# Kernel tuning notes

Measured on AMD Instinct MI355X. Metric: run time of the kernel, lower is better.

Reference implementation:

```python
import jax, jax.numpy as jnp
import numpy as np

B, N, F, D, KVQ, H, S, ITERS = 64, 4096, 256, 256, 256, 4, 8, 3
DH = KVQ // H
SCALE = DH ** -0.5
EPS = 1e-8
LN_EPS = 1e-5


def layernorm(x, w, b):
    m = jnp.mean(x, axis=-1, keepdims=True)
    v = jnp.var(x, axis=-1, keepdims=True)
    return (x - m) * jax.lax.rsqrt(v + LN_EPS) * w + b


def setup_inputs() -> dict:
    key = jax.random.key(0)
    ks = jax.random.split(key, 8)
    def init(k, shape, fan_in):
        return jax.random.normal(k, shape, dtype=jnp.float32) * (fan_in ** -0.5)
    return {
        "inputs": jax.random.normal(ks[0], (B, N, F), dtype=jnp.float32),
        "conditioning": jax.random.normal(ks[1], (B, S, D), dtype=jnp.float32),
        "ln_in_w": jnp.ones((F,), jnp.float32),
        "ln_in_b": jnp.zeros((F,), jnp.float32),
        "ln_s_w": jnp.ones((D,), jnp.float32),
        "ln_s_b": jnp.zeros((D,), jnp.float32),
        "wq": init(ks[2], (KVQ, D), D),
        "wk": init(ks[3], (KVQ, F), F),
        "wv": init(ks[4], (KVQ, F), F),
        "gru_wih": init(ks[5], (3 * D, KVQ), KVQ),
        "gru_whh": init(ks[6], (3 * D, D), D),
        "gru_bih": jnp.zeros((3 * D,), jnp.float32),
        "gru_bhh": jnp.zeros((3 * D,), jnp.float32),
    }


def gru_cell(x, h, wih, whh, bih, bhh):
    # x: [..., KVQ], h: [..., D]; torch.nn.GRUCell math
    gi = x @ wih.T + bih  # [..., 3D]
    gh = h @ whh.T + bhh
    i_r, i_z, i_n = jnp.split(gi, 3, axis=-1)
    h_r, h_z, h_n = jnp.split(gh, 3, axis=-1)
    r = jax.nn.sigmoid(i_r + h_r)
    z = jax.nn.sigmoid(i_z + h_z)
    n = jnp.tanh(i_n + r * h_n)
    return (1.0 - z) * n + z * h


def reference(inputs, conditioning, ln_in_w, ln_in_b, ln_s_w, ln_s_b, wq, wk, wv, gru_wih, gru_whh, gru_bih, gru_bhh):
    x = layernorm(inputs, ln_in_w, ln_in_b)  # [B,N,F]
    k = (x @ wk.T).reshape(B, N, H, DH)
    v = (x @ wv.T).reshape(B, N, H, DH)

    slots = conditioning
    attn_out = None
    for _ in range(ITERS):
        slots_prev = slots
        sn = layernorm(slots, ln_s_w, ln_s_b)
        q = (sn @ wq.T).reshape(B, S, H, DH)
        dots = jnp.einsum('bihd,bjhd->bihj', q, k) * SCALE  # [B,S,H,N]
        # inverted softmax: normalize over flattened (slot, head) axis
        attn = jax.nn.softmax(dots.reshape(B, S * H, N), axis=1).reshape(B, S, H, N)
        attn_before = attn
        attn = attn + EPS
        attn = attn / jnp.sum(attn, axis=-1, keepdims=True)
        updates = jnp.einsum('bjhd,bihj->bihd', v, attn).reshape(B, S, KVQ)
        slots = gru_cell(updates.reshape(-1, KVQ), slots_prev.reshape(-1, D),
                         gru_wih, gru_whh, gru_bih, gru_bhh).reshape(B, S, D)
        attn_out = jnp.mean(attn_before, axis=2)  # [B,S,N]
    return slots, attn_out
```

## Files before the change

kernel.cpp:

```cpp
#include <hip/hip_runtime.h>
#include <hip/hip_bf16.h>
#include <math.h>


using frag_ab = __attribute__((ext_vector_type(8))) short;
using f32x4  = __attribute__((ext_vector_type(4))) float;

__device__ __forceinline__ unsigned short f2bf(float f) {
  unsigned int x = __float_as_uint(f);
  x += 0x7fffu + ((x >> 16) & 1u);
  return (unsigned short)(x >> 16);
}
__device__ __forceinline__ float bf2f(unsigned short u) {
  return __uint_as_float((unsigned int)u << 16);
}
__device__ __forceinline__ float dot8(const uint4 w, const float* __restrict__ x) {
  return bf2f((unsigned short)(w.x & 0xffff)) * x[0] +
         bf2f((unsigned short)(w.x >> 16)) * x[1] +
         bf2f((unsigned short)(w.y & 0xffff)) * x[2] +
         bf2f((unsigned short)(w.y >> 16)) * x[3] +
         bf2f((unsigned short)(w.z & 0xffff)) * x[4] +
         bf2f((unsigned short)(w.z >> 16)) * x[5] +
         bf2f((unsigned short)(w.w & 0xffff)) * x[6] +
         bf2f((unsigned short)(w.w >> 16)) * x[7];
}

__global__ __launch_bounds__(256) void k_wcvt2(const float* __restrict__ wih,
                                               const float* __restrict__ whh,
                                               const float* __restrict__ wv,
                                               unsigned short* __restrict__ wihB,
                                               unsigned short* __restrict__ whhB,
                                               unsigned short* __restrict__ wvB) {
  const long idx = (long)blockIdx.x * 1024 + threadIdx.x * 4;
  const float* src;
  unsigned short* dst;
  long off;
  if (idx < 196608) { src = wih; dst = wihB; off = idx; }
  else if (idx < 393216) { src = whh; dst = whhB; off = idx - 196608; }
  else { src = wv; dst = wvB; off = idx - 393216; }
  const float4 v = *(const float4*)(src + off);
  uint2 o;
  o.x = (unsigned)f2bf(v.x) | ((unsigned)f2bf(v.y) << 16);
  o.y = (unsigned)f2bf(v.z) | ((unsigned)f2bf(v.w) << 16);
  *(uint2*)(dst + off) = o;
}

__global__ __launch_bounds__(256) void k_mprep(const float* __restrict__ wq,
                                               const float* __restrict__ wk,
                                               unsigned short* __restrict__ MTB) {
  const int f = blockIdx.x, h = blockIdx.y, D = threadIdx.x;
  float acc = 0.f;
#pragma unroll 8
  for (int d = 0; d < 64; ++d)
    acc += wq[(h * 64 + d) * 256 + D] * wk[(h * 64 + d) * 256 + f];
  MTB[((long)(h * 256 + f)) * 256 + D] = f2bf(acc * 0.125f);
}

__global__ __launch_bounds__(256) void k_precvt(
    const float* __restrict__ xsrc, const float* __restrict__ lnw,
    const float* __restrict__ lnb, unsigned short* __restrict__ Xh,
    unsigned short* __restrict__ XhT) {
  __shared__ __align__(16) unsigned short XT[256 * 68];
  const int t = threadIdx.x;
  const int lane = t & 63, w = t >> 6;
  const long row0 = (long)blockIdx.x * 64;
  const long b = row0 >> 12;
  const long j0 = row0 & 4095;

  float w4[4], b4[4];
#pragma unroll
  for (int k = 0; k < 4; ++k) {
    w4[k] = lnw[k * 64 + lane];
    b4[k] = lnb[k * 64 + lane];
  }
  for (int rr = 0; rr < 16; ++rr) {
    const long row = row0 + w * 16 + rr;
    float x[4];
    float s = 0.f, ss = 0.f;
#pragma unroll
    for (int k = 0; k < 4; ++k) {
      x[k] = xsrc[row * 256 + k * 64 + lane];
      s += x[k];
      ss += x[k] * x[k];
    }
#pragma unroll
    for (int m = 1; m < 64; m <<= 1) {
      s += __shfl_xor(s, m);
      ss += __shfl_xor(ss, m);
    }
    const float mean = s * (1.f / 256.f);
    const float rstd = rsqrtf(ss * (1.f / 256.f) - mean * mean + 1e-5f);
#pragma unroll
    for (int k = 0; k < 4; ++k) {
      const unsigned short u = f2bf((x[k] - mean) * rstd * w4[k] + b4[k]);
      Xh[row * 256 + k * 64 + lane] = u;
      *(unsigned short*)((char*)XT + (k * 64 + lane) * 136 + (w * 16 + rr) * 2) = u;
    }
  }
  __syncthreads();
#pragma unroll
  for (int fp = 0; fp < 4; ++fp) {
    const int f = fp * 64 + (t >> 2);
    const int jq = t & 3;
    uint2 v0 = *(const uint2*)((const char*)XT + f * 136 + jq * 32 + 0);
    uint2 v1 = *(const uint2*)((const char*)XT + f * 136 + jq * 32 + 8);
    uint2 v2 = *(const uint2*)((const char*)XT + f * 136 + jq * 32 + 16);
    uint2 v3 = *(const uint2*)((const char*)XT + f * 136 + jq * 32 + 24);
    unsigned short* dst = XhT + (b * 256 + f) * 4096 + j0 + jq * 16;
    *(uint4*)(dst) = make_uint4(v0.x, v0.y, v1.x, v1.y);
    *(uint4*)(dst + 8) = make_uint4(v2.x, v2.y, v3.x, v3.y);
  }
}

__global__ __launch_bounds__(256) void k_sv(const unsigned short* __restrict__ XhT,
                                            float* __restrict__ svx) {
  const int b = blockIdx.x >> 2, fq = blockIdx.x & 3;
  const int lane = threadIdx.x & 63, w = threadIdx.x >> 6;
  for (int rr = 0; rr < 16; ++rr) {
    const int f = fq * 64 + w * 16 + rr;
    const unsigned short* p = XhT + ((long)(b * 256 + f)) * 4096;
    float s = 0.f;
#pragma unroll
    for (int i = 0; i < 8; ++i) {
      const uint4 v = *(const uint4*)(p + i * 512 + lane * 8);
      s += bf2f((unsigned short)(v.x & 0xffff)) + bf2f((unsigned short)(v.x >> 16)) +
           bf2f((unsigned short)(v.y & 0xffff)) + bf2f((unsigned short)(v.y >> 16)) +
           bf2f((unsigned short)(v.z & 0xffff)) + bf2f((unsigned short)(v.z >> 16)) +
           bf2f((unsigned short)(v.w & 0xffff)) + bf2f((unsigned short)(v.w >> 16));
    }
#pragma unroll
    for (int m = 1; m < 64; m <<= 1) s += __shfl_xor(s, m);
    if (lane == 0) svx[b * 256 + f] = s;
  }
}

__global__ __launch_bounds__(256) void k_q(
    const float* __restrict__ slots, const float* __restrict__ lnw,
    const float* __restrict__ lnb, const unsigned short* __restrict__ MTB,
    unsigned short* __restrict__ qt) {
  __shared__ float sl[8 * 256];
  __shared__ float mstat[8], rstat[8];
  const int b = blockIdx.x, h = blockIdx.y, t = threadIdx.x;
#pragma unroll
  for (int i = 0; i < 8; ++i) sl[i * 256 + t] = slots[b * 2048 + i * 256 + t];
  __syncthreads();
  if (t < 8) {
    float s = 0.f, ss = 0.f;
    for (int k = 0; k < 256; ++k) {
      const float x = sl[t * 256 + k];
      s += x;
      ss += x * x;
    }
    const float m = s * (1.f / 256.f);
    mstat[t] = m;
    rstat[t] = rsqrtf(ss * (1.f / 256.f) - m * m + 1e-5f);
  }
  __syncthreads();
  const float w = lnw[t], bb = lnb[t];
#pragma unroll
  for (int i = 0; i < 8; ++i)
    sl[i * 256 + t] = (sl[i * 256 + t] - mstat[i]) * rstat[i] * w + bb;
  __syncthreads();
  float acc[8] = {};
  const uint4* mrow = (const uint4*)(MTB + ((long)(h * 256 + t)) * 256);
#pragma unroll 4
  for (int D8 = 0; D8 < 32; ++D8) {
    const uint4 m = mrow[D8];
#pragma unroll
    for (int i = 0; i < 8; ++i) acc[i] += dot8(m, sl + i * 256 + D8 * 8);
  }
#pragma unroll
  for (int i = 0; i < 8; ++i) {
    const int ih = i * 4 + h;
    *(unsigned short*)((char*)qt + b * 16384 + ih * 512 +
                       ((2 * t) ^ ((ih & 7) << 4))) = f2bf(acc[i]);
  }
}

template <bool LAST>
__global__ __launch_bounds__(256) void k_att(
    const unsigned short* __restrict__ qt, const unsigned short* __restrict__ Xh,
    const unsigned short* __restrict__ XhT, float* __restrict__ upart,
    float* __restrict__ rowsum_part, float* __restrict__ attn_out) {
  __shared__ __align__(16) unsigned short Qs[32 * 256];
  __shared__ __align__(16) unsigned short Ps[4][1024];
  __shared__ float ured[4][2048];
  __shared__ float wred[4][32];
  const int t = threadIdx.x;
  const int lane = t & 63, wid = t >> 6;
  const int li = lane & 15, kg = lane >> 4;
  const int b = blockIdx.y;
  const long j0 = (long)blockIdx.x * 512 + wid * 128;

#pragma unroll
  for (int rnd = 0; rnd < 4; ++rnd)
    __builtin_amdgcn_global_load_lds(
        (const unsigned int*)((const char*)qt + b * 16384 + rnd * 4096 + t * 16),
        (unsigned int*)((char*)Qs + rnd * 4096 + t * 16), 16, 0, 0);
  __syncthreads();

  float rsum0 = 0.f, rsum1 = 0.f;
  f32x4 pv[2][16];
#pragma unroll
  for (int s = 0; s < 2; ++s)
#pragma unroll
    for (int ft = 0; ft < 16; ++ft) pv[s][ft] = (f32x4){0.f, 0.f, 0.f, 0.f};

  unsigned short* Pw = Ps[wid];

  for (int ch = 0; ch < 4; ++ch) {
    const long jc = j0 + ch * 32;
    f32x4 dacc[2][2];
    dacc[0][0] = (f32x4){0.f, 0.f, 0.f, 0.f};
    dacc[0][1] = (f32x4){0.f, 0.f, 0.f, 0.f};
    dacc[1][0] = (f32x4){0.f, 0.f, 0.f, 0.f};
    dacc[1][1] = (f32x4){0.f, 0.f, 0.f, 0.f};
#pragma unroll
    for (int jsub = 0; jsub < 2; ++jsub) {
      frag_ab kf[8];
      const unsigned short* kp =
          Xh + ((long)b * 4096 + jc + jsub * 16 + li) * 256 + kg * 8;
#pragma unroll
      for (int ks = 0; ks < 8; ++ks) kf[ks] = *(const frag_ab*)(kp + ks * 32);
#pragma unroll
      for (int g = 0; g < 2; ++g) {
        const char* qrow = (const char*)Qs + (g * 16 + li) * 512;
        const int swz = (li & 7) << 4;
#pragma unroll
        for (int ks = 0; ks < 8; ++ks) {
          const frag_ab qf = *(const frag_ab*)(qrow + ((ks * 64 + kg * 16) ^ swz));
          dacc[jsub][g] = __builtin_amdgcn_mfma_f32_16x16x32_bf16(
              kf[ks], qf, dacc[jsub][g], 0, 0, 0);
        }
      }
    }
    float p[2][2][4];
#pragma unroll
    for (int jsub = 0; jsub < 2; ++jsub) {
#pragma unroll
      for (int r = 0; r < 4; ++r) {
        const float d0 = dacc[jsub][0][r];
        const float d1 = dacc[jsub][1][r];
        float mx = fmaxf(d0, d1);
        mx = fmaxf(mx, __shfl_xor(mx, 1));
        mx = fmaxf(mx, __shfl_xor(mx, 2));
        mx = fmaxf(mx, __shfl_xor(mx, 4));
        mx = fmaxf(mx, __shfl_xor(mx, 8));
        float e0 = __expf(d0 - mx), e1 = __expf(d1 - mx);
        float sm = e0 + e1;
        sm += __shfl_xor(sm, 1);
        sm += __shfl_xor(sm, 2);
        sm += __shfl_xor(sm, 4);
        sm += __shfl_xor(sm, 8);
        const float inv = 1.f / sm;
        e0 *= inv;
        e1 *= inv;
        p[jsub][0][r] = e0;
        p[jsub][1][r] = e1;
        rsum0 += e0;
        rsum1 += e1;
        if (LAST) {
          float s0 = e0 + __shfl_xor(e0, 1);
          s0 += __shfl_xor(s0, 2);
          float s1 = e1 + __shfl_xor(e1, 1);
          s1 += __shfl_xor(s1, 2);
          if ((li & 3) == 0) {
            const long jg = jc + jsub * 16 + kg * 4 + r;
            attn_out[((long)b * 8 + (li >> 2)) * 4096 + jg] = s0 * 0.25f;
            attn_out[((long)b * 8 + 4 + (li >> 2)) * 4096 + jg] = s1 * 0.25f;
          }
        }
      }
    }
    asm volatile("s_waitcnt lgkmcnt(0)" ::: "memory");
#pragma unroll
    for (int g = 0; g < 2; ++g) {
      const int ih = g * 16 + li;
      char* prow = (char*)Pw + ih * 64;
      const int swz = ((ih >> 2) & 3) << 4;
#pragma unroll
      for (int jsub = 0; jsub < 2; ++jsub)
#pragma unroll
        for (int rp = 0; rp < 2; ++rp) {
          const unsigned int pk =
              (unsigned)f2bf(p[jsub][g][2 * rp]) |
              ((unsigned)f2bf(p[jsub][g][2 * rp + 1]) << 16);
          const int jb = (jsub * 16 + kg * 4 + 2 * rp) * 2;
          *(unsigned int*)(prow + (jb ^ swz)) = pk;
        }
    }
    asm volatile("s_waitcnt lgkmcnt(0)" ::: "memory");
    const frag_ab pa0 = *(const frag_ab*)(
        (const char*)Pw + li * 64 + ((kg * 16) ^ (((li >> 2) & 3) << 4)));
    const frag_ab pa1 = *(const frag_ab*)(
        (const char*)Pw + (16 + li) * 64 +
        ((kg * 16) ^ ((((16 + li) >> 2) & 3) << 4)));
#pragma unroll
    for (int ft = 0; ft < 16; ++ft) {
      const frag_ab vf = *(const frag_ab*)(
          XhT + ((long)b * 256 + ft * 16 + li) * 4096 + jc + kg * 8);
      pv[0][ft] = __builtin_amdgcn_mfma_f32_16x16x32_bf16(pa0, vf, pv[0][ft], 0, 0, 0);
      pv[1][ft] = __builtin_amdgcn_mfma_f32_16x16x32_bf16(pa1, vf, pv[1][ft], 0, 0, 0);
    }
  }

  rsum0 += __shfl_xor(rsum0, 16);
  rsum0 += __shfl_xor(rsum0, 32);
  rsum1 += __shfl_xor(rsum1, 16);
  rsum1 += __shfl_xor(rsum1, 32);
  if (lane < 16) {
    wred[wid][lane] = rsum0;
    wred[wid][16 + lane] = rsum1;
  }

  const long pb = (long)blockIdx.x * 64 + b;
#pragma unroll
  for (int p4 = 0; p4 < 4; ++p4) {
    __syncthreads();
    if ((kg >> 1) == (p4 & 1)) {
#pragma unroll
      for (int ft = 0; ft < 16; ++ft)
#pragma unroll
        for (int r = 0; r < 4; ++r)
          ured[wid][((kg & 1) * 4 + r) * 256 + ft * 16 + li] = pv[p4 >> 1][ft][r];
    }
    __syncthreads();
#pragma unroll
    for (int o = 0; o < 8; ++o) {
      const int idx = o * 256 + t;
      upart[(pb * 32 + p4 * 8 + o) * 256 + t] =
          ured[0][idx] + ured[1][idx] + ured[2][idx] + ured[3][idx];
    }
  }
  if (t < 32)
    rowsum_part[pb * 32 + t] = wred[0][t] + wred[1][t] + wred[2][t] + wred[3][t];
}

__global__ __launch_bounds__(256) void k_xu(
    const float* __restrict__ upart, const float* __restrict__ svx,
    const float* __restrict__ rowsum_part, float* __restrict__ xu) {
  const int t = threadIdx.x;
  const int ih = blockIdx.x;
  const int b = blockIdx.y;
  float s2 = 0.f;
#pragma unroll
  for (int p = 0; p < 8; ++p)
    s2 += rowsum_part[((long)(p * 64 + b)) * 32 + ih];
  const float rs = 1.f / (s2 + 4096.f * 1e-8f);
  float pp = 0.f;
#pragma unroll
  for (int p = 0; p < 8; ++p)
    pp += upart[(((long)(p * 64 + b)) * 32 + ih) * 256 + t];
  xu[((long)(b * 32 + ih)) * 256 + t] = (pp + svx[b * 256 + t] * 1e-8f) * rs;
}

template <bool LAST>
__global__ __launch_bounds__(512, 4) void k_gq(
    const float* __restrict__ xu, const unsigned short* __restrict__ wvB,
    const unsigned short* __restrict__ wihB, const unsigned short* __restrict__ whhB,
    const float* __restrict__ bih, const float* __restrict__ bhh,
    const float* __restrict__ lnw, const float* __restrict__ lnb,
    const unsigned short* __restrict__ MTB, float* __restrict__ slots,
    unsigned short* __restrict__ qt, float* __restrict__ dout) {
  __shared__ float xul[4][256];
  __shared__ float hl[256];
  __shared__ float up2[2][256];
  __shared__ float updF[256];
  __shared__ float gI[3][256], gH[3][256];
  __shared__ float snl[256];
  __shared__ float mr[2];
  const int t = threadIdx.x;
  const int i = blockIdx.x;
  const int b = blockIdx.y;
  const int f = t & 255, half = t >> 8;

  if (t < 256) hl[t] = slots[b * 2048 + i * 256 + t];
#pragma unroll
  for (int hh = 0; hh < 2; ++hh) {
    const int row = half * 2 + hh;
    xul[row][f] = xu[((long)(b * 32 + i * 4 + row)) * 256 + f];
  }
  __syncthreads();
  {
    const float* xr = xul[f >> 6];
    const uint4* wr = (const uint4*)(wvB + (long)f * 256 + half * 128);
    float a = 0.f;
#pragma unroll 4
    for (int k8 = 0; k8 < 16; ++k8) a += dot8(wr[k8], xr + half * 128 + k8 * 8);
    up2[half][f] = a;
  }
  __syncthreads();
  if (t < 256) updF[t] = up2[0][t] + up2[1][t];
  __syncthreads();
  {
    const int c = t;
    const uint4* wi = (const uint4*)(wihB + (long)c * 256);
    const uint4* wh = (const uint4*)(whhB + (long)c * 256);
    float gi = 0.f, gh = 0.f;
#pragma unroll 4
    for (int k8 = 0; k8 < 32; ++k8) {
      gi += dot8(wi[k8], updF + k8 * 8);
      gh += dot8(wh[k8], hl + k8 * 8);
    }
    gI[c >> 8][c & 255] = gi + bih[c];
    gH[c >> 8][c & 255] = gh + bhh[c];
  }
  if (t < 256) {
    const int c = 512 + t;
    const uint4* wi = (const uint4*)(wihB + (long)c * 256);
    const uint4* wh = (const uint4*)(whhB + (long)c * 256);
    float gi = 0.f, gh = 0.f;
#pragma unroll 4
    for (int k8 = 0; k8 < 32; ++k8) {
      gi += dot8(wi[k8], updF + k8 * 8);
      gh += dot8(wh[k8], hl + k8 * 8);
    }
    gI[2][t] = gi + bih[c];
    gH[2][t] = gh + bhh[c];
  }
  __syncthreads();
  if (t < 256) {
    const float r = 1.f / (1.f + __expf(-(gI[0][t] + gH[0][t])));
    const float z = 1.f / (1.f + __expf(-(gI[1][t] + gH[1][t])));
    const float n = tanhf(gI[2][t] + r * gH[2][t]);
    const float hn = (1.f - z) * n + z * hl[t];
    slots[b * 2048 + i * 256 + t] = hn;
    if (LAST) dout[b * 2048 + i * 256 + t] = hn;
    xul[0][t] = hn;
  }
  if (LAST) return;
  __syncthreads();
  if (t < 64) {
    float s = 0.f, ss = 0.f;
#pragma unroll
    for (int u = 0; u < 4; ++u) {
      const float x = xul[0][u * 64 + t];
      s += x;
      ss += x * x;
    }
#pragma unroll
    for (int m = 1; m < 64; m <<= 1) {
      s += __shfl_xor(s, m);
      ss += __shfl_xor(ss, m);
    }
    if (t == 0) {
      const float mn = s * (1.f / 256.f);
      mr[0] = mn;
      mr[1] = rsqrtf(ss * (1.f / 256.f) - mn * mn + 1e-5f);
    }
  }
  __syncthreads();
  if (t < 256) snl[t] = (xul[0][t] - mr[0]) * mr[1] * lnw[t] + lnb[t];
  __syncthreads();
#pragma unroll
  for (int hh = 0; hh < 2; ++hh) {
    const int h = half * 2 + hh;
    const uint4* m = (const uint4*)(MTB + ((long)(h * 256 + f)) * 256);
    float acc = 0.f;
#pragma unroll 4
    for (int D8 = 0; D8 < 32; ++D8) acc += dot8(m[D8], snl + D8 * 8);
    const int ih = i * 4 + h;
    *(unsigned short*)((char*)qt + b * 16384 + ih * 512 +
                       ((2 * f) ^ ((ih & 7) << 4))) = f2bf(acc);
  }
}

extern "C" void kernel_launch(void* const* d_in, const int* in_sizes, int n_in,
                              void* d_out, int out_size, void* d_ws,
                              size_t ws_size, hipStream_t stream) {
  const float* xin = (const float*)d_in[0];
  const float* cond = (const float*)d_in[1];
  const float* lnin_w = (const float*)d_in[2];
  const float* lnin_b = (const float*)d_in[3];
  const float* lns_w = (const float*)d_in[4];
  const float* lns_b = (const float*)d_in[5];
  const float* wq = (const float*)d_in[6];
  const float* wk = (const float*)d_in[7];
  const float* wv = (const float*)d_in[8];
  const float* gwih = (const float*)d_in[9];
  const float* gwhh = (const float*)d_in[10];
  const float* gbih = (const float*)d_in[11];
  const float* gbhh = (const float*)d_in[12];
  float* out = (float*)d_out;

  char* ws = (char*)d_ws;
  unsigned short* Xh = (unsigned short*)ws;   ws += 262144l * 256 * 2;
  unsigned short* XhT = (unsigned short*)ws;  ws += 64l * 256 * 4096 * 2;
  unsigned short* MTB = (unsigned short*)ws;  ws += 4l * 256 * 256 * 2;
  unsigned short* qt = (unsigned short*)ws;   ws += 64l * 32 * 256 * 2;
  float* upart = (float*)ws;                  ws += 8l * 64 * 32 * 256 * 4;
  float* svx = (float*)ws;                    ws += 64l * 256 * 4;
  float* rowsum_part = (float*)ws;            ws += 8l * 64 * 32 * 4;
  float* xu = (float*)ws;                     ws += 64l * 32 * 256 * 4;
  float* slots = (float*)ws;                  ws += 512l * 256 * 4;
  unsigned short* wihB = (unsigned short*)ws; ws += 768l * 256 * 2;
  unsigned short* whhB = (unsigned short*)ws; ws += 768l * 256 * 2;
  unsigned short* wvB = (unsigned short*)ws;  ws += 256l * 256 * 2;

  hipMemcpyAsync(slots, cond, 512 * 256 * 4, hipMemcpyDeviceToDevice, stream);
  k_wcvt2<<<448, 256, 0, stream>>>(gwih, gwhh, wv, wihB, whhB, wvB);
  k_mprep<<<dim3(256, 4), 256, 0, stream>>>(wq, wk, MTB);
  k_precvt<<<4096, 256, 0, stream>>>(xin, lnin_w, lnin_b, Xh, XhT);
  k_sv<<<256, 256, 0, stream>>>(XhT, svx);
  k_q<<<dim3(64, 4), 256, 0, stream>>>(slots, lns_w, lns_b, MTB, qt);

  k_att<false><<<dim3(8, 64), 256, 0, stream>>>(qt, Xh, XhT, upart,
                                                rowsum_part, out + 131072);
  k_xu<<<dim3(32, 64), 256, 0, stream>>>(upart, svx, rowsum_part, xu);
  k_gq<false><<<dim3(8, 64), 512, 0, stream>>>(xu, wvB, wihB, whhB, gbih, gbhh,
                                               lns_w, lns_b, MTB, slots, qt, out);
  k_att<false><<<dim3(8, 64), 256, 0, stream>>>(qt, Xh, XhT, upart,
                                                rowsum_part, out + 131072);
  k_xu<<<dim3(32, 64), 256, 0, stream>>>(upart, svx, rowsum_part, xu);
  k_gq<false><<<dim3(8, 64), 512, 0, stream>>>(xu, wvB, wihB, whhB, gbih, gbhh,
                                               lns_w, lns_b, MTB, slots, qt, out);
  k_att<true><<<dim3(8, 64), 256, 0, stream>>>(qt, Xh, XhT, upart,
                                               rowsum_part, out + 131072);
  k_xu<<<dim3(32, 64), 256, 0, stream>>>(upart, svx, rowsum_part, xu);
  k_gq<true><<<dim3(8, 64), 512, 0, stream>>>(xu, wvB, wihB, whhB, gbih, gbhh,
                                              lns_w, lns_b, MTB, slots, qt, out);
}
```

Baseline: 655.1 us.

## Fuse column-sum into layernorm prepass and fold xu reduction into GRU kernel

The per-feature column sums of the normalized inputs are now accumulated inside the layernorm/transpose kernel as per-block partials. A tiny reduction kernel combines them, replacing a separate pass that re-read the whole transposed bf16 tensor. The k_xu kernel, launched once per iteration, is removed and its partial-sum reduction and normalization move into the GRU/query kernel, saving three launches and an intermediate buffer. tanhf is replaced with an exp-based approximation, and the column sums now come from fp32 values rather than bf16-rounded ones.

After: 629.0 us. 4.0% less time.

```diff
diff --git a/kernel.cpp b/kernel.cpp
--- a/kernel.cpp
+++ b/kernel.cpp
@@ -23,6 +23,11 @@
          bf2f((unsigned short)(w.z >> 16)) * x[5] +
          bf2f((unsigned short)(w.w & 0xffff)) * x[6] +
          bf2f((unsigned short)(w.w >> 16)) * x[7];
+}
+__device__ __forceinline__ float fast_tanh(float x) {
+  const float xc = fminf(fmaxf(x, -15.f), 15.f);
+  const float e2 = __expf(2.f * xc);
+  return (e2 - 1.f) / (e2 + 1.f);
 }
 
 __global__ __launch_bounds__(256) void k_wcvt2(const float* __restrict__ wih,
@@ -59,8 +64,9 @@
 __global__ __launch_bounds__(256) void k_precvt(
     const float* __restrict__ xsrc, const float* __restrict__ lnw,
     const float* __restrict__ lnb, unsigned short* __restrict__ Xh,
-    unsigned short* __restrict__ XhT) {
+    unsigned short* __restrict__ XhT, float* __restrict__ svp) {
   __shared__ __align__(16) unsigned short XT[256 * 68];
+  __shared__ float svred[4][256];
   const int t = threadIdx.x;
   const int lane = t & 63, w = t >> 6;
   const long row0 = (long)blockIdx.x * 64;
@@ -73,6 +79,7 @@
     w4[k] = lnw[k * 64 + lane];
     b4[k] = lnb[k * 64 + lane];
   }
+  float sacc[4] = {0.f, 0.f, 0.f, 0.f};
   for (int rr = 0; rr < 16; ++rr) {
     const long row = row0 + w * 16 + rr;
     float x[4];
@@ -92,12 +99,18 @@
     const float rstd = rsqrtf(ss * (1.f / 256.f) - mean * mean + 1e-5f);
 #pragma unroll
     for (int k = 0; k < 4; ++k) {
-      const unsigned short u = f2bf((x[k] - mean) * rstd * w4[k] + b4[k]);
+      const float xl = (x[k] - mean) * rstd * w4[k] + b4[k];
+      sacc[k] += xl;
+      const unsigned short u = f2bf(xl);
       Xh[row * 256 + k * 64 + lane] = u;
       *(unsigned short*)((char*)XT + (k * 64 + lane) * 136 + (w * 16 + rr) * 2) = u;
     }
   }
-  __syncthreads();
+#pragma unroll
+  for (int k = 0; k < 4; ++k) svred[w][k * 64 + lane] = sacc[k];
+  __syncthreads();
+  svp[(long)blockIdx.x * 256 + t] =
+      svred[0][t] + svred[1][t] + svred[2][t] + svred[3][t];
 #pragma unroll
   for (int fp = 0; fp < 4; ++fp) {
     const int f = fp * 64 + (t >> 2);
@@ -112,26 +125,13 @@
   }
 }
 
-__global__ __launch_bounds__(256) void k_sv(const unsigned short* __restrict__ XhT,
-                                            float* __restrict__ svx) {
-  const int b = blockIdx.x >> 2, fq = blockIdx.x & 3;
-  const int lane = threadIdx.x & 63, w = threadIdx.x >> 6;
-  for (int rr = 0; rr < 16; ++rr) {
-    const int f = fq * 64 + w * 16 + rr;
-    const unsigned short* p = XhT + ((long)(b * 256 + f)) * 4096;
-    float s = 0.f;
-#pragma unroll
-    for (int i = 0; i < 8; ++i) {
-      const uint4 v = *(const uint4*)(p + i * 512 + lane * 8);
-      s += bf2f((unsigned short)(v.x & 0xffff)) + bf2f((unsigned short)(v.x >> 16)) +
-           bf2f((unsigned short)(v.y & 0xffff)) + bf2f((unsigned short)(v.y >> 16)) +
-           bf2f((unsigned short)(v.z & 0xffff)) + bf2f((unsigned short)(v.z >> 16)) +
-           bf2f((unsigned short)(v.w & 0xffff)) + bf2f((unsigned short)(v.w >> 16));
-    }
-#pragma unroll
-    for (int m = 1; m < 64; m <<= 1) s += __shfl_xor(s, m);
-    if (lane == 0) svx[b * 256 + f] = s;
-  }
+__global__ __launch_bounds__(256) void k_svr(const float* __restrict__ svp,
+                                             float* __restrict__ svx) {
+  const int b = blockIdx.x, t = threadIdx.x;
+  float s = 0.f;
+#pragma unroll 8
+  for (int c = 0; c < 64; ++c) s += svp[((long)(b * 64 + c)) * 256 + t];
+  svx[b * 256 + t] = s;
 }
 
 __global__ __launch_bounds__(256) void k_q(
@@ -336,27 +336,10 @@
     rowsum_part[pb * 32 + t] = wred[0][t] + wred[1][t] + wred[2][t] + wred[3][t];
 }
 
-__global__ __launch_bounds__(256) void k_xu(
-    const float* __restrict__ upart, const float* __restrict__ svx,
-    const float* __restrict__ rowsum_part, float* __restrict__ xu) {
-  const int t = threadIdx.x;
-  const int ih = blockIdx.x;
-  const int b = blockIdx.y;
-  float s2 = 0.f;
-#pragma unroll
-  for (int p = 0; p < 8; ++p)
-    s2 += rowsum_part[((long)(p * 64 + b)) * 32 + ih];
-  const float rs = 1.f / (s2 + 4096.f * 1e-8f);
-  float pp = 0.f;
-#pragma unroll
-  for (int p = 0; p < 8; ++p)
-    pp += upart[(((long)(p * 64 + b)) * 32 + ih) * 256 + t];
-  xu[((long)(b * 32 + ih)) * 256 + t] = (pp + svx[b * 256 + t] * 1e-8f) * rs;
-}
-
 template <bool LAST>
 __global__ __launch_bounds__(512, 4) void k_gq(
-    const float* __restrict__ xu, const unsigned short* __restrict__ wvB,
+    const float* __restrict__ upart, const float* __restrict__ svx,
+    const float* __restrict__ rowsum_part, const unsigned short* __restrict__ wvB,
     const unsigned short* __restrict__ wihB, const unsigned short* __restrict__ whhB,
     const float* __restrict__ bih, const float* __restrict__ bhh,
     const float* __restrict__ lnw, const float* __restrict__ lnb,
@@ -375,10 +358,21 @@
   const int f = t & 255, half = t >> 8;
 
   if (t < 256) hl[t] = slots[b * 2048 + i * 256 + t];
+  const float svf = svx[b * 256 + f] * 1e-8f;
 #pragma unroll
   for (int hh = 0; hh < 2; ++hh) {
     const int row = half * 2 + hh;
-    xul[row][f] = xu[((long)(b * 32 + i * 4 + row)) * 256 + f];
+    const int ih = i * 4 + row;
+    float s2 = 0.f;
+#pragma unroll
+    for (int p = 0; p < 8; ++p)
+      s2 += rowsum_part[((long)(p * 64 + b)) * 32 + ih];
+    const float rs = 1.f / (s2 + 4096.f * 1e-8f);
+    float pp = 0.f;
+#pragma unroll
+    for (int p = 0; p < 8; ++p)
+      pp += upart[(((long)(p * 64 + b)) * 32 + ih) * 256 + f];
+    xul[row][f] = (pp + svf) * rs;
   }
   __syncthreads();
   {
@@ -422,7 +416,7 @@
   if (t < 256) {
     const float r = 1.f / (1.f + __expf(-(gI[0][t] + gH[0][t])));
     const float z = 1.f / (1.f + __expf(-(gI[1][t] + gH[1][t])));
-    const float n = tanhf(gI[2][t] + r * gH[2][t]);
+    const float n = fast_tanh(gI[2][t] + r * gH[2][t]);
     const float hn = (1.f - z) * n + z * hl[t];
     slots[b * 2048 + i * 256 + t] = hn;
     if (LAST) dout[b * 2048 + i * 256 + t] = hn;
@@ -489,9 +483,9 @@
   unsigned short* MTB = (unsigned short*)ws;  ws += 4l * 256 * 256 * 2;
   unsigned short* qt = (unsigned short*)ws;   ws += 64l * 32 * 256 * 2;
   float* upart = (float*)ws;                  ws += 8l * 64 * 32 * 256 * 4;
+  float* svp = (float*)ws;                    ws += 4096l * 256 * 4;
   float* svx = (float*)ws;                    ws += 64l * 256 * 4;
   float* rowsum_part = (float*)ws;            ws += 8l * 64 * 32 * 4;
-  float* xu = (float*)ws;                     ws += 64l * 32 * 256 * 4;
   float* slots = (float*)ws;                  ws += 512l * 256 * 4;
   unsigned short* wihB = (unsigned short*)ws; ws += 768l * 256 * 2;
   unsigned short* whhB = (unsigned short*)ws; ws += 768l * 256 * 2;
@@ -500,23 +494,23 @@
   hipMemcpyAsync(slots, cond, 512 * 256 * 4, hipMemcpyDeviceToDevice, stream);
   k_wcvt2<<<448, 256, 0, stream>>>(gwih, gwhh, wv, wihB, whhB, wvB);
   k_mprep<<<dim3(256, 4), 256, 0, stream>>>(wq, wk, MTB);
-  k_precvt<<<4096, 256, 0, stream>>>(xin, lnin_w, lnin_b, Xh, XhT);
-  k_sv<<<256, 256, 0, stream>>>(XhT, svx);
+  k_precvt<<<4096, 256, 0, stream>>>(xin, lnin_w, lnin_b, Xh, XhT, svp);
+  k_svr<<<64, 256, 0, stream>>>(svp, svx);
   k_q<<<dim3(64, 4), 256, 0, stream>>>(slots, lns_w, lns_b, MTB, qt);
 
   k_att<false><<<dim3(8, 64), 256, 0, stream>>>(qt, Xh, XhT, upart,
                                                 rowsum_part, out + 131072);
-  k_xu<<<dim3(32, 64), 256, 0, stream>>>(upart, svx, rowsum_part, xu);
-  k_gq<false><<<dim3(8, 64), 512, 0, stream>>>(xu, wvB, wihB, whhB, gbih, gbhh,
-                                               lns_w, lns_b, MTB, slots, qt, out);
+  k_gq<false><<<dim3(8, 64), 512, 0, stream>>>(upart, svx, rowsum_part, wvB,
+                                               wihB, whhB, gbih, gbhh, lns_w,
+                                               lns_b, MTB, slots, qt, out);
   k_att<false><<<dim3(8, 64), 256, 0, stream>>>(qt, Xh, XhT, upart,
                                                 rowsum_part, out + 131072);
-  k_xu<<<dim3(32, 64), 256, 0, stream>>>(upart, svx, rowsum_part, xu);
-  k_gq<false><<<dim3(8, 64), 512, 0, stream>>>(xu, wvB, wihB, whhB, gbih, gbhh,
-                                               lns_w, lns_b, MTB, slots, qt, out);
+  k_gq<false><<<dim3(8, 64), 512, 0, stream>>>(upart, svx, rowsum_part, wvB,
+                                               wihB, whhB, gbih, gbhh, lns_w,
+                                               lns_b, MTB, slots, qt, out);
   k_att<true><<<dim3(8, 64), 256, 0, stream>>>(qt, Xh, XhT, upart,
                                                rowsum_part, out + 131072);
-  k_xu<<<dim3(32, 64), 256, 0, stream>>>(upart, svx, rowsum_part, xu);
-  k_gq<true><<<dim3(8, 64), 512, 0, stream>>>(xu, wvB, wihB, whhB, gbih, gbhh,
-                                              lns_w, lns_b, MTB, slots, qt, out);
-}
+  k_gq<true><<<dim3(8, 64), 512, 0, stream>>>(upart, svx, rowsum_part, wvB,
+                                              wihB, whhB, gbih, gbhh, lns_w,
+                                              lns_b, MTB, slots, qt, out);
+}
```
